# Performance work log

Hardware: AMD Instinct MI355X
Metric: run time of the kernel (lower is better)

The kernel has to match this reference:

```python
import jax, jax.numpy as jnp
import numpy as np

N_NODES = 100000
IN_CH = 512
OUT_CH = 64
N_EDGES = 1600000
NEG_SLOPE = 0.2  # PyG GATv2Conv default negative_slope


def setup_inputs() -> dict:
    key = jax.random.key(0)
    ks = jax.random.split(key, 8)
    x = jax.random.normal(ks[0], (N_NODES, IN_CH), dtype=jnp.float32)
    edge_index = jax.random.randint(ks[1], (2, N_EDGES), 0, N_NODES, dtype=jnp.int64)
    s_in = 1.0 / np.sqrt(IN_CH)
    s_out = 1.0 / np.sqrt(OUT_CH)
    W_l = jax.random.uniform(ks[2], (IN_CH, OUT_CH), jnp.float32, -s_in, s_in)
    b_l = jnp.zeros((OUT_CH,), jnp.float32)
    W_r = jax.random.uniform(ks[3], (IN_CH, OUT_CH), jnp.float32, -s_in, s_in)
    b_r = jnp.zeros((OUT_CH,), jnp.float32)
    att = jax.random.uniform(ks[4], (OUT_CH,), jnp.float32, -s_out, s_out)
    bias = jnp.zeros((OUT_CH,), jnp.float32)
    return {"x": x, "edge_index": edge_index, "W_l": W_l, "b_l": b_l,
            "W_r": W_r, "b_r": b_r, "att": att, "bias": bias}


def reference(x, edge_index, W_l, b_l, W_r, b_r, att, bias):
    n = x.shape[0]
    # add self loops (PyG GATv2Conv default add_self_loops=True)
    loop = jnp.arange(n, dtype=edge_index.dtype)
    src = jnp.concatenate([edge_index[0], loop])  # source j
    dst = jnp.concatenate([edge_index[1], loop])  # target i

    x_l = x @ W_l + b_l  # [N, D] source-side transform
    x_r = x @ W_r + b_r  # [N, D] target-side transform

    # GATv2 attention logit per edge: att . LeakyReLU(x_l[j] + x_r[i])
    z = x_l[src] + x_r[dst]                       # [E, D]
    z = jnp.where(z > 0, z, NEG_SLOPE * z)
    logits = z @ att                               # [E]

    # segment softmax over incoming edges of each target node
    seg_max = jax.ops.segment_max(logits, dst, num_segments=n)
    seg_max = jnp.where(jnp.isfinite(seg_max), seg_max, 0.0)
    e = jnp.exp(logits - seg_max[dst])
    denom = jax.ops.segment_sum(e, dst, num_segments=n)
    alpha = e / jnp.maximum(denom[dst], 1e-16)     # [E]

    # weighted scatter-add aggregation of source features
    out = jax.ops.segment_sum(alpha[:, None] * x_l[src], dst, num_segments=n)
    return out + bias
```

## Files before the change

kernel.cpp:

```cpp
#include <hip/hip_runtime.h>
#include <hip/hip_bf16.h>

constexpr int IC = 512;
constexpr int OC = 64;
#define NEG_SLOPE 0.2f

constexpr int EPB = 4096;
constexpr int NBK = 128;
constexpr int BKSHIFT = 10;
constexpr int BKSIZE = 1024;

typedef __attribute__((ext_vector_type(8))) __bf16 bf16x8;
typedef __attribute__((ext_vector_type(4))) float f32x4;
typedef __attribute__((ext_vector_type(8))) unsigned short u16x8;
typedef unsigned short u16;

__device__ __forceinline__ float bf2f(u16 h) {
  return __uint_as_float(((unsigned)h) << 16);
}

__global__ __launch_bounds__(256)
void k_shuffleB(const float* __restrict__ Wl, const float* __restrict__ Wr,
                __hip_bfloat16* __restrict__ Bp) {
  const int tid = blockIdx.x * 256 + threadIdx.x;
  if (tid >= 8 * 16 * 64) return;
  const int lane = tid & 63;
  const int kb = (tid >> 6) & 15;
  const int cb = tid >> 10;
  const int col = cb * 16 + (lane & 15);
  const int k0 = kb * 32 + (lane >> 4) * 8;
  const float* W = (col < OC) ? (Wl + col) : (Wr + (col - OC));
  bf16x8 v;
  #pragma unroll
  for (int j = 0; j < 8; ++j) v[j] = (__bf16)W[(size_t)(k0 + j) * OC];
  *(bf16x8*)(Bp + (size_t)tid * 8) = v;
}

__device__ inline bf16x8 cvt8(const float4& a, const float4& b) {
  bf16x8 r;
  r[0] = (__bf16)a.x; r[1] = (__bf16)a.y; r[2] = (__bf16)a.z; r[3] = (__bf16)a.w;
  r[4] = (__bf16)b.x; r[5] = (__bf16)b.y; r[6] = (__bf16)b.z; r[7] = (__bf16)b.w;
  return r;
}

__device__ __forceinline__ void gload_lds16(const float* g, const float* l) {
  __builtin_amdgcn_global_load_lds(
      (const __attribute__((address_space(1))) float*)(uintptr_t)g,
      (__attribute__((address_space(3))) float*)(uintptr_t)l,
      16, 0, 0);
}

__global__ __launch_bounds__(256)
void k_gemm(const float* __restrict__ x, const __hip_bfloat16* __restrict__ Bp,
            const float* __restrict__ bl, const float* __restrict__ br,
            __bf16* __restrict__ xl, __bf16* __restrict__ xr, int n) {
  __shared__ float As[2][128 * 64];
  const int t = threadIdx.x;
  const int lane = t & 63;
  const int w = t >> 6;
  const int l15 = lane & 15, lg = lane >> 4;
  const int rowbase_g = blockIdx.x * 128 + w * 32;

  const float* srcp[8];
  #pragma unroll
  for (int j = 0; j < 8; ++j) {
    const int row_l = w * 32 + j * 4 + lg;
    const int grow = min(blockIdx.x * 128 + row_l, n - 1);
    const int gch = l15 ^ ((j * 4 + lg) & 15);
    srcp[j] = x + (size_t)grow * IC + gch * 4;
  }
  const bf16x8* pb = (const bf16x8*)Bp + lane;

  f32x4 acc[2][8] = {};

  #pragma unroll
  for (int j = 0; j < 8; ++j)
    gload_lds16(srcp[j], &As[0][w * 2048 + j * 256]);

  int buf = 0;
  for (int kt = 0; kt < 8; ++kt) {
    bf16x8 bfr[2][8];
    #pragma unroll
    for (int kb = 0; kb < 2; ++kb)
      #pragma unroll
      for (int cb = 0; cb < 8; ++cb)
        bfr[kb][cb] = pb[(cb * 16 + kt * 2 + kb) * 64];
    asm volatile("s_waitcnt vmcnt(16)" ::: "memory");
    if (kt < 7) {
      #pragma unroll
      for (int j = 0; j < 8; ++j)
        gload_lds16(srcp[j] + (kt + 1) * 64, &As[buf ^ 1][w * 2048 + j * 256]);
    }
    #pragma unroll
    for (int kb = 0; kb < 2; ++kb) {
      const int kc0 = kb * 8 + lg * 2;
      const int s0 = (kc0 ^ l15) * 4;
      const int s1 = ((kc0 + 1) ^ l15) * 4;
      #pragma unroll
      for (int rg = 0; rg < 2; ++rg) {
        const int rbase = (w * 32 + rg * 16 + l15) * 64;
        const float4 f0 = *(const float4*)&As[buf][rbase + s0];
        const float4 f1 = *(const float4*)&As[buf][rbase + s1];
        const bf16x8 af = cvt8(f0, f1);
        #pragma unroll
        for (int cb = 0; cb < 8; ++cb)
          acc[rg][cb] = __builtin_amdgcn_mfma_f32_16x16x32_bf16(af, bfr[kb][cb], acc[rg][cb], 0, 0, 0);
      }
    }
    buf ^= 1;
  }

  #pragma unroll
  for (int cb = 0; cb < 8; ++cb) {
    const int col = cb * 16 + l15;
    __bf16* dst = (col < OC) ? xl : xr;
    const int c2 = col & (OC - 1);
    const float bv = (col < OC) ? bl[c2] : br[c2];
    #pragma unroll
    for (int rg = 0; rg < 2; ++rg) {
      const int rb = rowbase_g + rg * 16 + lg * 4;
      #pragma unroll
      for (int q = 0; q < 4; ++q)
        if (rb + q < n) dst[(size_t)(rb + q) * OC + c2] = (__bf16)(acc[rg][cb][q] + bv);
    }
  }
}

__global__ __launch_bounds__(256)
void k_bin1a(const int* __restrict__ edst, int* __restrict__ slen,
             int E, int nch) {
  __shared__ int lcnt[NBK];
  const int t = threadIdx.x;
  const int c = blockIdx.x;
  const int e0 = c * EPB;
  if (t < NBK) lcnt[t] = 0;
  __syncthreads();
  #pragma unroll
  for (int j = 0; j < 16; ++j) {
    const int i = e0 + j * 256 + t;
    if (i < E) atomicAdd(&lcnt[edst[i] >> BKSHIFT], 1);
  }
  __syncthreads();
  if (t < NBK) slen[t * nch + c] = lcnt[t];
}

__global__ __launch_bounds__(256)
void k_colscan(int* __restrict__ slen, int* __restrict__ btot, int nch) {
  __shared__ int sm[256];
  const int t = threadIdx.x;
  const int base = blockIdx.x * nch;
  const int per = (nch + 255) / 256;
  int v[8];
  int s = 0;
  for (int k = 0; k < per; ++k) {
    const int idx = t * per + k;
    v[k] = (idx < nch) ? slen[base + idx] : 0;
    s += v[k];
  }
  sm[t] = s;
  __syncthreads();
  #pragma unroll
  for (int d = 1; d < 256; d <<= 1) {
    int u = (t >= d) ? sm[t - d] : 0;
    __syncthreads();
    sm[t] += u;
    __syncthreads();
  }
  int run = (t == 0) ? 0 : sm[t - 1];
  for (int k = 0; k < per; ++k) {
    const int idx = t * per + k;
    if (idx < nch) slen[base + idx] = run;
    run += v[k];
  }
  if (t == 255) btot[blockIdx.x] = sm[255];
}

__global__ __launch_bounds__(256)
void k_bscan(const int* __restrict__ btot, int* __restrict__ bbase, int nbk) {
  __shared__ int sm[256];
  const int t = threadIdx.x;
  const int v = (t < nbk) ? btot[t] : 0;
  sm[t] = v;
  __syncthreads();
  #pragma unroll
  for (int d = 1; d < 256; d <<= 1) {
    int u = (t >= d) ? sm[t - d] : 0;
    __syncthreads();
    sm[t] += u;
    __syncthreads();
  }
  if (t < NBK) bbase[t] = sm[t] - v;
  if (t == NBK - 1) bbase[NBK] = sm[t];
}

__global__ __launch_bounds__(256)
void k_bin1b(const int* __restrict__ esrc, const int* __restrict__ edst,
             const int* __restrict__ slen, const int* __restrict__ bbase,
             int* __restrict__ bstage, int E, int nch) {
  __shared__ int lcnt[NBK];
  __shared__ int lbase[NBK];
  __shared__ int ldst[NBK];
  __shared__ int lword[EPB];
  __shared__ unsigned char lbkt[EPB];
  __shared__ int sm[256];
  const int t = threadIdx.x;
  const int c = blockIdx.x;
  const int e0 = c * EPB;
  if (t < NBK) lcnt[t] = 0;
  __syncthreads();

  int s_[16], d_[16], r_[16];
  #pragma unroll
  for (int j = 0; j < 16; ++j) {
    const int i = e0 + j * 256 + t;
    if (i < E) {
      s_[j] = esrc[i];
      d_[j] = edst[i];
      r_[j] = atomicAdd(&lcnt[d_[j] >> BKSHIFT], 1);
    }
  }
  __syncthreads();
  const int vv = (t < NBK) ? lcnt[t] : 0;
  sm[t] = vv;
  __syncthreads();
  #pragma unroll
  for (int d = 1; d < 256; d <<= 1) {
    int u = (t >= d) ? sm[t - d] : 0;
    __syncthreads();
    sm[t] += u;
    __syncthreads();
  }
  if (t < NBK) {
    lbase[t] = sm[t] - vv;
    ldst[t] = bbase[t] + slen[t * nch + c];
  }
  __syncthreads();
  #pragma unroll
  for (int j = 0; j < 16; ++j) {
    const int i = e0 + j * 256 + t;
    if (i < E) {
      const int b = d_[j] >> BKSHIFT;
      const int pos = lbase[b] + r_[j];
      lword[pos] = (s_[j] << BKSHIFT) | (d_[j] & (BKSIZE - 1));
      lbkt[pos] = (unsigned char)b;
    }
  }
  __syncthreads();
  const int used = min(E - e0, EPB);
  for (int k = t; k < used; k += 256) {
    const int b = lbkt[k];
    bstage[ldst[b] + (k - lbase[b])] = lword[k];
  }
}

__global__ __launch_bounds__(1024)
void k_boffplace(const int* __restrict__ bstage, const int* __restrict__ bbase,
                 int* __restrict__ off, int* __restrict__ rec, int n, int nbk) {
  __shared__ int lc[BKSIZE];
  __shared__ int sw[16];
  const int t = threadIdx.x;
  const int b = blockIdx.x;
  const int node0 = b << BKSHIFT;
  lc[t] = 0;
  __syncthreads();
  const int beg = bbase[b];
  const int end = bbase[b + 1];
  for (int k = beg + t; k < end; k += 1024)
    atomicAdd(&lc[bstage[k] & (BKSIZE - 1)], 1);
  __syncthreads();
  const int v = lc[t];
  int sc = v;
  #pragma unroll
  for (int d = 1; d < 64; d <<= 1) {
    const int u = __shfl_up(sc, d);
    if ((t & 63) >= d) sc += u;
  }
  if ((t & 63) == 63) sw[t >> 6] = sc;
  __syncthreads();
  if (t < 64) {
    int s2 = (t < 16) ? sw[t] : 0;
    #pragma unroll
    for (int d = 1; d < 16; d <<= 1) {
      const int u = __shfl_up(s2, d);
      if (t >= d) s2 += u;
    }
    if (t < 16) sw[t] = s2;
  }
  __syncthreads();
  const int wbase = (t >= 64) ? sw[(t >> 6) - 1] : 0;
  const int node = node0 + t;
  int o = 0;
  if (node < n) {
    o = beg + node0 + t + (wbase + sc - v);
    off[node] = o;
    rec[o] = node;
  }
  if (b == nbk - 1 && t == 1023) off[n] = bbase[nbk] + n;
  lc[t] = o + 1;
  __syncthreads();
  for (int k = beg + t; k < end; k += 1024) {
    const int w = bstage[k];
    const int pos = atomicAdd(&lc[w & (BKSIZE - 1)], 1);
    rec[pos] = w >> BKSHIFT;
  }
}

__global__ __launch_bounds__(256)
void k_gather(const int* __restrict__ off, const int* __restrict__ rec,
              const u16* __restrict__ xl, const u16* __restrict__ xr,
              const float* __restrict__ att, const float* __restrict__ bias,
              float* __restrict__ out, int n) {
  const int lane = threadIdx.x & 63;
  const int node = (blockIdx.x * 256 + threadIdx.x) >> 6;
  if (node >= n) return;
  const int slot = lane >> 3;
  const int c8 = (lane & 7) * 8;

  const u16x8 xrh = *(const u16x8*)(xr + (size_t)node * OC + c8);
  float xrv[8], aw[8];
  #pragma unroll
  for (int j = 0; j < 8; ++j) {
    xrv[j] = bf2f(xrh[j]);
    aw[j] = att[c8 + j];
  }

  const int beg = off[node];
  const int end = off[node + 1];
  float denom = 0.0f;
  float acc[8] = {};

  for (int c0 = beg; c0 < end; c0 += 64) {
    const int cend = min(end - c0, 64);
    int myrec = 0;
    if (lane < cend) myrec = rec[c0 + lane];
    int eidx = slot;
    bool v = (eidx < cend);
    int s = __shfl(myrec, eidx);
    u16x8 xh = {};
    if (v) xh = *(const u16x8*)(xl + (size_t)s * OC + c8);
    for (int m = 0; m * 8 < cend; ++m) {
      const u16x8 ch = xh;
      const bool curv = v;
      eidx += 8;
      v = (eidx < cend);
      s = __shfl(myrec, min(eidx, 63));
      if (v) xh = *(const u16x8*)(xl + (size_t)s * OC + c8);
      float cur[8];
      float lg = 0.0f;
      #pragma unroll
      for (int j = 0; j < 8; ++j) {
        cur[j] = bf2f(ch[j]);
        float z = cur[j] + xrv[j];
        z = z > 0.0f ? z : NEG_SLOPE * z;
        lg = fmaf(z, aw[j], lg);
      }
      lg += __shfl_xor(lg, 1);
      lg += __shfl_xor(lg, 2);
      lg += __shfl_xor(lg, 4);
      const float wgt = curv ? __expf(lg) : 0.0f;
      denom += wgt;
      #pragma unroll
      for (int j = 0; j < 8; ++j) acc[j] = fmaf(wgt, cur[j], acc[j]);
    }
  }
  denom += __shfl_xor(denom, 8);
  denom += __shfl_xor(denom, 16);
  denom += __shfl_xor(denom, 32);
  #pragma unroll
  for (int j = 0; j < 8; ++j) {
    acc[j] += __shfl_xor(acc[j], 8);
    acc[j] += __shfl_xor(acc[j], 16);
    acc[j] += __shfl_xor(acc[j], 32);
  }

  if (slot == 0) {
    const float inv = 1.0f / denom;
    float4 o0, o1;
    o0.x = acc[0] * inv + bias[c8 + 0];
    o0.y = acc[1] * inv + bias[c8 + 1];
    o0.z = acc[2] * inv + bias[c8 + 2];
    o0.w = acc[3] * inv + bias[c8 + 3];
    o1.x = acc[4] * inv + bias[c8 + 4];
    o1.y = acc[5] * inv + bias[c8 + 5];
    o1.z = acc[6] * inv + bias[c8 + 6];
    o1.w = acc[7] * inv + bias[c8 + 7];
    *(float4*)(out + (size_t)node * OC + c8) = o0;
    *(float4*)(out + (size_t)node * OC + c8 + 4) = o1;
  }
}

extern "C" void kernel_launch(void* const* d_in, const int* in_sizes, int n_in,
                              void* d_out, int out_size, void* d_ws, size_t ws_size,
                              hipStream_t stream) {
  const float* x    = (const float*)d_in[0];
  const int*   ei   = (const int*)d_in[1];
  const float* Wl   = (const float*)d_in[2];
  const float* bl   = (const float*)d_in[3];
  const float* Wr   = (const float*)d_in[4];
  const float* br   = (const float*)d_in[5];
  const float* att  = (const float*)d_in[6];
  const float* bias = (const float*)d_in[7];
  float* out = (float*)d_out;

  const int n = in_sizes[0] / IC;
  const int E = in_sizes[1] / 2;
  const int total = E + n;
  const int* esrc = ei;
  const int* edst = ei + E;
  const int nch = (E + EPB - 1) / EPB;
  const int nbk = (n + BKSIZE - 1) >> BKSHIFT;

  char* wp = (char*)d_ws;
  __hip_bfloat16* Bp = (__hip_bfloat16*)wp;  wp += 131072;
  __bf16* xl  = (__bf16*)wp;                 wp += (size_t)n * OC * 2;
  __bf16* xr  = (__bf16*)wp;                 wp += (size_t)n * OC * 2;
  int* bstage = (int*)wp;                    wp += (size_t)E * 4;
  int* slen   = (int*)wp;                    wp += (size_t)NBK * nch * 4;
  int* btot   = (int*)wp;                    wp += (size_t)NBK * 4;
  int* bbase  = (int*)wp;                    wp += (size_t)(NBK + 1) * 4;
  int* off    = (int*)wp;                    wp += (size_t)(n + 1) * 4;
  int* rec    = (int*)wp;                    wp += (size_t)total * 4;

  k_shuffleB<<<32, 256, 0, stream>>>(Wl, Wr, Bp);
  k_gemm<<<(n + 127) / 128, 256, 0, stream>>>(x, Bp, bl, br, xl, xr, n);
  k_bin1a<<<nch, 256, 0, stream>>>(edst, slen, E, nch);
  k_colscan<<<nbk, 256, 0, stream>>>(slen, btot, nch);
  k_bscan<<<1, 256, 0, stream>>>(btot, bbase, nbk);
  k_bin1b<<<nch, 256, 0, stream>>>(esrc, edst, slen, bbase, bstage, E, nch);
  k_boffplace<<<nbk, 1024, 0, stream>>>(bstage, bbase, off, rec, n, nbk);
  k_gather<<<((size_t)n * 64 + 255) / 256, 256, 0, stream>>>(off, rec, (const u16*)xl, (const u16*)xr, att, bias, out, n);
}
```

Measured before the change: 169.3 us.

## Fuse edge binning into GEMM launch and replace two-pass binning with regroup

```diff
diff --git a/kernel.cpp b/kernel.cpp
--- a/kernel.cpp
+++ b/kernel.cpp
@@ -51,21 +51,81 @@
 }
 
 __global__ __launch_bounds__(256)
-void k_gemm(const float* __restrict__ x, const __hip_bfloat16* __restrict__ Bp,
-            const float* __restrict__ bl, const float* __restrict__ br,
-            __bf16* __restrict__ xl, __bf16* __restrict__ xr, int n) {
-  __shared__ float As[2][128 * 64];
+void k_gemm_bin(const float* __restrict__ x, const __hip_bfloat16* __restrict__ Bp,
+                const float* __restrict__ bl, const float* __restrict__ br,
+                __bf16* __restrict__ xl, __bf16* __restrict__ xr, int n,
+                const int* __restrict__ esrc, const int* __restrict__ edst,
+                int* __restrict__ slen, int* __restrict__ sbase,
+                int* __restrict__ stage, int E, int nch) {
+  __shared__ char smem[65536];
+  const int i = blockIdx.x;
   const int t = threadIdx.x;
+  const bool isbin = ((i % 3) == 2) && ((i / 3) < nch);
+
+  if (isbin) {
+    int* lcnt  = (int*)smem;
+    int* lbase = lcnt + NBK;
+    int* sm    = lbase + NBK;
+    int* lword = sm + 256;
+    const int c = i / 3;
+    const int e0 = c * EPB;
+    if (t < NBK) lcnt[t] = 0;
+    __syncthreads();
+    int s_[16], d_[16], r_[16];
+    #pragma unroll
+    for (int j = 0; j < 16; ++j) {
+      const int ii = e0 + j * 256 + t;
+      if (ii < E) {
+        s_[j] = esrc[ii];
+        d_[j] = edst[ii];
+        r_[j] = atomicAdd(&lcnt[d_[j] >> BKSHIFT], 1);
+      }
+    }
+    __syncthreads();
+    const int vv = (t < NBK) ? lcnt[t] : 0;
+    sm[t] = vv;
+    __syncthreads();
+    #pragma unroll
+    for (int d = 1; d < 256; d <<= 1) {
+      int u = (t >= d) ? sm[t - d] : 0;
+      __syncthreads();
+      sm[t] += u;
+      __syncthreads();
+    }
+    if (t < NBK) {
+      const int lb = sm[t] - vv;
+      lbase[t] = lb;
+      sbase[c * NBK + t] = lb;
+      slen[t * nch + c] = vv;
+    }
+    __syncthreads();
+    #pragma unroll
+    for (int j = 0; j < 16; ++j) {
+      const int ii = e0 + j * 256 + t;
+      if (ii < E) {
+        const int b = d_[j] >> BKSHIFT;
+        lword[lbase[b] + r_[j]] = (s_[j] << BKSHIFT) | (d_[j] & (BKSIZE - 1));
+      }
+    }
+    __syncthreads();
+    const int used = min(E - e0, EPB);
+    for (int k = t; k < used; k += 256)
+      stage[(size_t)c * EPB + k] = lword[k];
+    return;
+  }
+
+  float (*As)[128 * 64] = (float (*)[128 * 64])smem;
+  const int g = i - min(i / 3, nch);
   const int lane = t & 63;
   const int w = t >> 6;
   const int l15 = lane & 15, lg = lane >> 4;
-  const int rowbase_g = blockIdx.x * 128 + w * 32;
+  const int rowbase_g = g * 128 + w * 32;
 
   const float* srcp[8];
   #pragma unroll
   for (int j = 0; j < 8; ++j) {
     const int row_l = w * 32 + j * 4 + lg;
-    const int grow = min(blockIdx.x * 128 + row_l, n - 1);
+    const int grow = min(g * 128 + row_l, n - 1);
     const int gch = l15 ^ ((j * 4 + lg) & 15);
     srcp[j] = x + (size_t)grow * IC + gch * 4;
   }
@@ -124,24 +184,6 @@
         if (rb + q < n) dst[(size_t)(rb + q) * OC + c2] = (__bf16)(acc[rg][cb][q] + bv);
     }
   }
-}
-
-__global__ __launch_bounds__(256)
-void k_bin1a(const int* __restrict__ edst, int* __restrict__ slen,
-             int E, int nch) {
-  __shared__ int lcnt[NBK];
-  const int t = threadIdx.x;
-  const int c = blockIdx.x;
-  const int e0 = c * EPB;
-  if (t < NBK) lcnt[t] = 0;
-  __syncthreads();
-  #pragma unroll
-  for (int j = 0; j < 16; ++j) {
-    const int i = e0 + j * 256 + t;
-    if (i < E) atomicAdd(&lcnt[edst[i] >> BKSHIFT], 1);
-  }
-  __syncthreads();
-  if (t < NBK) slen[t * nch + c] = lcnt[t];
 }
 
 __global__ __launch_bounds__(256)
@@ -194,62 +236,28 @@
 }
 
 __global__ __launch_bounds__(256)
-void k_bin1b(const int* __restrict__ esrc, const int* __restrict__ edst,
-             const int* __restrict__ slen, const int* __restrict__ bbase,
-             int* __restrict__ bstage, int E, int nch) {
-  __shared__ int lcnt[NBK];
-  __shared__ int lbase[NBK];
-  __shared__ int ldst[NBK];
-  __shared__ int lword[EPB];
-  __shared__ unsigned char lbkt[EPB];
-  __shared__ int sm[256];
+void k_regroup(const int* __restrict__ stage, const int* __restrict__ sbase,
+               const int* __restrict__ colpref, const int* __restrict__ bbase,
+               int* __restrict__ bstage, int E, int nch, int nbk) {
+  __shared__ int sb[NBK + 1];
+  __shared__ int dbase[NBK];
+  const int c = blockIdx.x;
   const int t = threadIdx.x;
-  const int c = blockIdx.x;
-  const int e0 = c * EPB;
-  if (t < NBK) lcnt[t] = 0;
-  __syncthreads();
-
-  int s_[16], d_[16], r_[16];
-  #pragma unroll
-  for (int j = 0; j < 16; ++j) {
-    const int i = e0 + j * 256 + t;
-    if (i < E) {
-      s_[j] = esrc[i];
-      d_[j] = edst[i];
-      r_[j] = atomicAdd(&lcnt[d_[j] >> BKSHIFT], 1);
-    }
-  }
-  __syncthreads();
-  const int vv = (t < NBK) ? lcnt[t] : 0;
-  sm[t] = vv;
-  __syncthreads();
-  #pragma unroll
-  for (int d = 1; d < 256; d <<= 1) {
-    int u = (t >= d) ? sm[t - d] : 0;
-    __syncthreads();
-    sm[t] += u;
-    __syncthreads();
-  }
+  const int used = min(E - c * EPB, EPB);
   if (t < NBK) {
-    lbase[t] = sm[t] - vv;
-    ldst[t] = bbase[t] + slen[t * nch + c];
-  }
-  __syncthreads();
-  #pragma unroll
-  for (int j = 0; j < 16; ++j) {
-    const int i = e0 + j * 256 + t;
-    if (i < E) {
-      const int b = d_[j] >> BKSHIFT;
-      const int pos = lbase[b] + r_[j];
-      lword[pos] = (s_[j] << BKSHIFT) | (d_[j] & (BKSIZE - 1));
-      lbkt[pos] = (unsigned char)b;
-    }
-  }
-  __syncthreads();
-  const int used = min(E - e0, EPB);
+    sb[t] = sbase[c * NBK + t];
+    dbase[t] = (t < nbk) ? (bbase[t] + colpref[t * nch + c]) : 0;
+  }
+  if (t == 0) sb[NBK] = used;
+  __syncthreads();
   for (int k = t; k < used; k += 256) {
-    const int b = lbkt[k];
-    bstage[ldst[b] + (k - lbase[b])] = lword[k];
+    const int e = stage[(size_t)c * EPB + k];
+    int lo = 0, hi = NBK;
+    while (hi - lo > 1) {
+      const int mid = (lo + hi) >> 1;
+      if (sb[mid] <= k) lo = mid; else hi = mid;
+    }
+    bstage[dbase[lo] + (k - sb[lo])] = e;
   }
 }
 
@@ -409,24 +417,27 @@
   const int* edst = ei + E;
   const int nch = (E + EPB - 1) / EPB;
   const int nbk = (n + BKSIZE - 1) >> BKSHIFT;
+  const int gb = (n + 127) / 128;
 
   char* wp = (char*)d_ws;
   __hip_bfloat16* Bp = (__hip_bfloat16*)wp;  wp += 131072;
-  __bf16* xl  = (__bf16*)wp;                 wp += (size_t)n * OC * 2;
-  __bf16* xr  = (__bf16*)wp;                 wp += (size_t)n * OC * 2;
-  int* bstage = (int*)wp;                    wp += (size_t)E * 4;
-  int* slen   = (int*)wp;                    wp += (size_t)NBK * nch * 4;
-  int* btot   = (int*)wp;                    wp += (size_t)NBK * 4;
-  int* bbase  = (int*)wp;                    wp += (size_t)(NBK + 1) * 4;
-  int* off    = (int*)wp;                    wp += (size_t)(n + 1) * 4;
-  int* rec    = (int*)wp;                    wp += (size_t)total * 4;
+  __bf16* xl   = (__bf16*)wp;                wp += (size_t)n * OC * 2;
+  __bf16* xr   = (__bf16*)wp;                wp += (size_t)n * OC * 2;
+  int* stage   = (int*)wp;                   wp += (size_t)nch * EPB * 4;
+  int* bstage  = (int*)wp;                   wp += (size_t)E * 4;
+  int* slen    = (int*)wp;                   wp += (size_t)NBK * nch * 4;
+  int* sbase   = (int*)wp;                   wp += (size_t)nch * NBK * 4;
+  int* btot    = (int*)wp;                   wp += (size_t)NBK * 4;
+  int* bbase   = (int*)wp;                   wp += (size_t)(NBK + 1) * 4;
+  int* off     = (int*)wp;                   wp += (size_t)(n + 1) * 4;
+  int* rec     = (int*)wp;                   wp += (size_t)total * 4;
 
   k_shuffleB<<<32, 256, 0, stream>>>(Wl, Wr, Bp);
-  k_gemm<<<(n + 127) / 128, 256, 0, stream>>>(x, Bp, bl, br, xl, xr, n);
-  k_bin1a<<<nch, 256, 0, stream>>>(edst, slen, E, nch);
+  k_gemm_bin<<<gb + nch, 256, 0, stream>>>(x, Bp, bl, br, xl, xr, n,
+                                           esrc, edst, slen, sbase, stage, E, nch);
   k_colscan<<<nbk, 256, 0, stream>>>(slen, btot, nch);
   k_bscan<<<1, 256, 0, stream>>>(btot, bbase, nbk);
-  k_bin1b<<<nch, 256, 0, stream>>>(esrc, edst, slen, bbase, bstage, E, nch);
+  k_regroup<<<nch, 256, 0, stream>>>(stage, sbase, slen, bbase, bstage, E, nch, nbk);
   k_boffplace<<<nbk, 1024, 0, stream>>>(bstage, bbase, off, rec, n, nbk);
   k_gather<<<((size_t)n * 64 + 255) / 256, 256, 0, stream>>>(off, rec, (const u16*)xl, (const u16*)xr, att, bias, out, n);
 }
```

After: 171.4 us. Within noise of the previous version (+1.3%).
